# Performance work log

Measured on AMD Instinct MI355X. Metric: run time of the kernel, lower is better.

Reference implementation:

```python
import jax, jax.numpy as jnp
import numpy as np

N_HEADS = 16
PROJ_DIM = 64  # per-head dim
DIM = N_HEADS * PROJ_DIM  # 1024


def setup_inputs() -> dict:
    key = jax.random.key(0)
    k1, k2, k3, k4, k5 = jax.random.split(key, 5)
    N, L = 2, 2048
    scale = 1.0 / np.sqrt(DIM)
    return {
        "query": jax.random.normal(k1, (N, L, DIM), dtype=jnp.float32),
        "key": jax.random.normal(k2, (N, L, DIM), dtype=jnp.float32),
        "Wq": jax.random.normal(k3, (DIM, DIM), dtype=jnp.float32) * scale,
        "Wk": jax.random.normal(k4, (DIM, DIM), dtype=jnp.float32) * scale,
        "Wv": jax.random.normal(k5, (DIM, DIM), dtype=jnp.float32) * scale,
    }


def reference(query, key, Wq, Wk, Wv):
    # Causal linear-complexity attention (mask=True branch, left_first=False).
    N, Lq, _ = query.shape
    Lk = key.shape[1]
    H, Dh = N_HEADS, PROJ_DIM
    # torch Linear: x @ W.T ; reshape to (N, H, L, Dh)
    q = (query @ Wq.T).reshape(N, Lq, H, Dh).transpose(0, 2, 1, 3)
    k = (key @ Wk.T).reshape(N, Lk, H, Dh).transpose(0, 2, 1, 3)
    v = (key @ Wv.T).reshape(N, Lk, H, Dh).transpose(0, 2, 1, 3)
    q = jax.nn.softmax(q, axis=-1)
    k = jax.nn.softmax(k, axis=-1)
    # right[t] = sum_{s<=t} k_s^T v_s  : (N,H,Lk,Dh,Dh) cumulative outer products
    S = jnp.cumsum(jnp.einsum('nhti,nhtj->nhtij', k, v), axis=2)
    out = jnp.einsum('nhti,nhtij->nhtj', q, S)  # (N,H,Lq,Dh)
    return out.transpose(0, 2, 1, 3).reshape(N, Lq, H * Dh)
```

## Files before the change

### kernel.cpp

```cpp
#include <hip/hip_runtime.h>


constexpr int DIM  = 1024;
constexpr int H    = 16;
constexpr int DH   = 64;
constexpr int LSEQ = 2048;
constexpr int NB   = 2;
constexpr int MTOK = NB * LSEQ;
constexpr int CS   = 64;
constexpr int NC   = LSEQ / CS;
constexpr int SEG  = 8;
constexpr int CPS  = NC / SEG;

typedef __bf16 bf16x8 __attribute__((ext_vector_type(8)));
typedef float floatx4 __attribute__((ext_vector_type(4)));
typedef unsigned short ushort_t;

__device__ __forceinline__ ushort_t f2bf(float f) {
  unsigned int u = __float_as_uint(f);
  u += 0x7FFFu + ((u >> 16) & 1u);
  return (ushort_t)(u >> 16);
}

__device__ __forceinline__ void async16(void* lds, const void* g) {
  __builtin_amdgcn_global_load_lds(
      (const __attribute__((address_space(1))) unsigned int*)g,
      (__attribute__((address_space(3))) unsigned int*)lds, 16, 0, 0);
}

__device__ __forceinline__ bf16x8 tfrag(const unsigned int* T, int row, int uoff) {
  union { bf16x8 v; unsigned int u[4]; } r;
  const unsigned int* p = T + row * 33 + uoff;
  r.u[0] = p[0]; r.u[1] = p[1]; r.u[2] = p[2]; r.u[3] = p[3];
  return r.v;
}

__device__ __forceinline__ void transpose_tile(const ushort_t* g, unsigned int* TT, int tid) {
  const int ic = tid & 7, tp = tid >> 3;
  const ushort_t* r0 = g + (size_t)(2 * tp) * DIM + ic * 8;
  union { uint4 q; ushort_t u[8]; } a0, a1;
  a0.q = *(const uint4*)r0;
  a1.q = *(const uint4*)(r0 + DIM);
#pragma unroll
  for (int j = 0; j < 8; j++)
    TT[(8 * ic + j) * 33 + tp] = (unsigned int)a0.u[j] | ((unsigned int)a1.u[j] << 16);
}

__global__ __launch_bounds__(256) void cast_all(const float* __restrict__ q,
                                                const float* __restrict__ k,
                                                const float* __restrict__ wq,
                                                const float* __restrict__ wk,
                                                const float* __restrict__ wv,
                                                ushort_t* __restrict__ xbf,
                                                ushort_t* __restrict__ wbf) {
  const int seg = blockIdx.y;
  const float* src;
  ushort_t* dst;
  int n4;
  if (seg == 0)      { src = q;  dst = xbf;                  n4 = (4 << 20) / 4; }
  else if (seg == 1) { src = k;  dst = xbf + (4 << 20);      n4 = (4 << 20) / 4; }
  else if (seg == 2) { src = wq; dst = wbf;                  n4 = (1 << 20) / 4; }
  else if (seg == 3) { src = wk; dst = wbf + (1 << 20);      n4 = (1 << 20) / 4; }
  else               { src = wv; dst = wbf + (2 << 20);      n4 = (1 << 20) / 4; }
  for (int i = blockIdx.x * 256 + threadIdx.x; i < n4; i += gridDim.x * 256) {
    const float4 f = ((const float4*)src)[i];
    ((ushort4*)dst)[i] = make_ushort4(f2bf(f.x), f2bf(f.y), f2bf(f.z), f2bf(f.w));
  }
}

__global__ __launch_bounds__(512, 2) void gemm_fused(const ushort_t* __restrict__ xbf,
                                                     const ushort_t* __restrict__ wbf,
                                                     ushort_t* __restrict__ qp,
                                                     ushort_t* __restrict__ kp,
                                                     ushort_t* __restrict__ vp) {
  __shared__ __align__(16) ushort_t sh[65536];
  const int tid = threadIdx.x;

  const int xcd   = blockIdx.x & 7;
  const int local = blockIdx.x >> 3;
  const int T     = xcd * 24 + local;
  const int z     = T >> 6;
  const int rem   = T & 63;
  const int bm    = (rem >> 2) * 256;
  const int bn    = (rem & 3) * 256;

  const ushort_t* A = xbf + (z ? (size_t)(4 << 20) : 0);
  const ushort_t* W = wbf + (size_t)z * (1 << 20);
  ushort_t* C = (z == 0) ? qp : ((z == 1) ? kp : vp);

  const int lane  = tid & 63;
  const int wid   = tid >> 6;
  const int wr    = wid >> 2, wc = wid & 3;
  const int row16 = lane & 15, quad = lane >> 4;

  floatx4 acc[8][4] = {};

  const int srow = tid >> 3;
  const int lc   = (tid & 7) ^ (srow & 7);
  const ushort_t* pA[2][2];
  const ushort_t* pB[2][2];
#pragma unroll
  for (int h = 0; h < 2; h++)
#pragma unroll
    for (int rnd = 0; rnd < 2; rnd++) {
      pA[h][rnd] = A + (size_t)(bm + h * 128 + rnd * 64 + srow) * DIM + lc * 8;
      pB[h][rnd] = W + (size_t)(bn + h * 128 + rnd * 64 + srow) * DIM + lc * 8;
    }
  char* shW = (char*)sh;

#define STG(b, ism, h, kt)                                          \
  {                                                                 \
    char* d_ = shW + (b) * 65536 + (ism) * 32768 + (h) * 16384 + tid * 16; \
    async16(d_,        ((ism) ? pB : pA)[h][0] + (size_t)(kt) * 64);       \
    async16(d_ + 8192, ((ism) ? pB : pA)[h][1] + (size_t)(kt) * 64);       \
  }

  const int key = row16 & 7;
  const int xc0 = (quad ^ key) * 16;
  const int xc1 = ((4 + quad) ^ key) * 16;
  const int aOff = wr * 16384 + row16 * 128;
  const int bOff = 32768 + (wc >> 1) * 16384 + (wc & 1) * 8192 + row16 * 128;
  const char* shR = (const char*)sh;

  bf16x8 aF[4][2], bF[4][2];

#define RD_A4(p, base)                                                        \
  {                                                                           \
    _Pragma("unroll")                                                         \
    for (int mt = 0; mt < 4; mt++) {                                          \
      aF[mt][0] = *(const bf16x8*)(shR + (p) * 65536 + aOff + ((base) + mt) * 2048 + xc0); \
      aF[mt][1] = *(const bf16x8*)(shR + (p) * 65536 + aOff + ((base) + mt) * 2048 + xc1); \
    }                                                                         \
  }
#define RD_B2(p, base)                                                        \
  {                                                                           \
    _Pragma("unroll")                                                         \
    for (int j = 0; j < 2; j++) {                                             \
      bF[(base) + j][0] = *(const bf16x8*)(shR + (p) * 65536 + bOff + ((base) + j) * 2048 + xc0); \
      bF[(base) + j][1] = *(const bf16x8*)(shR + (p) * 65536 + bOff + ((base) + j) * 2048 + xc1); \
    }                                                                         \
  }
#define MFMA8(mb, nb)                                                         \
  {                                                                           \
    _Pragma("unroll")                                                         \
    for (int mt = 0; mt < 4; mt++)                                            \
      _Pragma("unroll")                                                       \
      for (int nt = 0; nt < 2; nt++) {                                        \
        acc[(mb) + mt][(nb) + nt] = __builtin_amdgcn_mfma_f32_16x16x32_bf16(  \
            aF[mt][0], bF[(nb) + nt][0], acc[(mb) + mt][(nb) + nt], 0, 0, 0); \
        acc[(mb) + mt][(nb) + nt] = __builtin_amdgcn_mfma_f32_16x16x32_bf16(  \
            aF[mt][1], bF[(nb) + nt][1], acc[(mb) + mt][(nb) + nt], 0, 0, 0); \
      }                                                                       \
  }
#define BARD()  asm volatile("s_barrier" ::: "memory")
#define LGKM0() asm volatile("s_waitcnt lgkmcnt(0)" ::: "memory")

  STG(0, 0, 0, 0); STG(0, 1, 0, 0);
  STG(0, 1, 1, 0); STG(0, 0, 1, 0);
  STG(1, 0, 0, 1); STG(1, 1, 0, 1);
  asm volatile("s_waitcnt vmcnt(4)" ::: "memory");
  BARD();

  for (int u = 0; u < 16; ++u) {
    const int p  = u & 1;
    const int qb = p ^ 1;
    RD_A4(p, 0); RD_B2(p, 0);
    if (u + 1 < 16) { STG(qb, 1, 1, u + 1); STG(qb, 0, 1, u + 1); }
    BARD(); LGKM0();
    __builtin_amdgcn_s_setprio(1); MFMA8(0, 0); __builtin_amdgcn_s_setprio(0);
    BARD();
    RD_B2(p, 2);
    BARD(); LGKM0();
    __builtin_amdgcn_s_setprio(1); MFMA8(0, 2); __builtin_amdgcn_s_setprio(0);
    BARD();
    RD_A4(p, 4);
    BARD(); LGKM0();
    __builtin_amdgcn_s_setprio(1); MFMA8(4, 0); __builtin_amdgcn_s_setprio(0);
    BARD();
    if (u + 2 < 16) {
      STG(p, 0, 0, u + 2); STG(p, 1, 0, u + 2);
      asm volatile("s_waitcnt vmcnt(4)" ::: "memory");
    } else {
      asm volatile("s_waitcnt vmcnt(0)" ::: "memory");
    }
    BARD();
    __builtin_amdgcn_s_setprio(1); MFMA8(4, 2); __builtin_amdgcn_s_setprio(0);
    BARD();
  }
#undef STG
#undef RD_A4
#undef RD_B2
#undef MFMA8
#undef BARD
#undef LGKM0
  __syncthreads();

  if (z < 2) {
#pragma unroll
    for (int mt = 0; mt < 8; mt++)
#pragma unroll
      for (int r = 0; r < 4; r++) {
        float m = fmaxf(fmaxf(acc[mt][0][r], acc[mt][1][r]),
                        fmaxf(acc[mt][2][r], acc[mt][3][r]));
#pragma unroll
        for (int o = 1; o < 16; o <<= 1) m = fmaxf(m, __shfl_xor(m, o, 64));
        float e[4], s = 0.f;
#pragma unroll
        for (int nt = 0; nt < 4; nt++) { e[nt] = __expf(acc[mt][nt][r] - m); s += e[nt]; }
#pragma unroll
        for (int o = 1; o < 16; o <<= 1) s += __shfl_xor(s, o, 64);
        const float inv = 1.f / s;
#pragma unroll
        for (int nt = 0; nt < 4; nt++) acc[mt][nt][r] = e[nt] * inv;
      }
  }

  ushort_t* CsB = sh;
#pragma unroll
  for (int p4 = 0; p4 < 4; ++p4) {
    __syncthreads();
    if (wr == (p4 >> 1)) {
      const int mh = (p4 & 1) * 4;
#pragma unroll
      for (int m4 = 0; m4 < 4; m4++)
#pragma unroll
        for (int nt = 0; nt < 4; nt++)
#pragma unroll
          for (int r = 0; r < 4; r++)
            CsB[(m4 * 16 + quad * 4 + r) * 264 + wc * 64 + nt * 16 + row16] =
                f2bf(acc[mh + m4][nt][r]);
    }
    __syncthreads();
#pragma unroll
    for (int it = 0; it < 4; it++) {
      const int ch = tid + it * 512;
      const int row = ch >> 5, ic = ch & 31;
      *(uint4*)&C[(size_t)(bm + p4 * 64 + row) * DIM + bn + ic * 8] =
          *(const uint4*)&CsB[row * 264 + ic * 8];
    }
  }
}

__global__ __launch_bounds__(1024, 1) void seg_T(const ushort_t* __restrict__ kp,
                                                 const ushort_t* __restrict__ vp,
                                                 float* __restrict__ cs,
                                                 float* __restrict__ segtot) {
  __shared__ unsigned int KT[4][64 * 33];
  __shared__ unsigned int VT[4][64 * 33];
  __shared__ float Tsl[3][DH * DH];
  const int s = blockIdx.x, h = blockIdx.y, n = blockIdx.z;
  const int tid = threadIdx.x;
  const int qd  = tid >> 8;
  const int t8  = tid & 255;
  const int lane = tid & 63;
  const int wid  = (tid >> 6) & 3;
  const int row16 = lane & 15, quad = lane >> 4;
  const int nh = n * H + h;
  const int c  = s * CPS + qd;
  const size_t gbase = ((size_t)(n * LSEQ + c * CS)) * DIM + h * DH;

  transpose_tile(kp + gbase, KT[qd], t8);
  transpose_tile(vp + gbase, VT[qd], t8);
  __syncthreads();

  floatx4 tacc[4] = {};
#pragma unroll
  for (int ks = 0; ks < 2; ks++) {
    const bf16x8 a = tfrag(VT[qd], wid * 16 + row16, ks * 16 + quad * 4);
#pragma unroll
    for (int nt = 0; nt < 4; nt++) {
      const bf16x8 b = tfrag(KT[qd], nt * 16 + row16, ks * 16 + quad * 4);
      tacc[nt] = __builtin_amdgcn_mfma_f32_16x16x32_bf16(a, b, tacc[nt], 0, 0, 0);
    }
  }
  if (qd < 3) {
#pragma unroll
    for (int nt = 0; nt < 4; nt++)
#pragma unroll
      for (int r = 0; r < 4; r++)
        Tsl[qd][(wid * 16 + quad * 4 + r) * DH + nt * 16 + row16] = tacc[nt][r];
  }
  __syncthreads();

  float* outp = cs + ((size_t)(nh * NC + c)) * (DH * DH);
#pragma unroll
  for (int nt = 0; nt < 4; nt++)
#pragma unroll
    for (int r = 0; r < 4; r++) {
      const int pos = (wid * 16 + quad * 4 + r) * DH + nt * 16 + row16;
      float p = 0.f;
      if (qd > 0) p += Tsl[0][pos];
      if (qd > 1) p += Tsl[1][pos];
      if (qd > 2) p += Tsl[2][pos];
      outp[pos] = p;
      if (qd == 3) {
        segtot[((size_t)(nh * SEG + s)) * (DH * DH) + pos] = p + tacc[nt][r];
      }
    }
}

__global__ __launch_bounds__(1024, 1) void attn2(const ushort_t* __restrict__ qp,
                                                 const ushort_t* __restrict__ kp,
                                                 const ushort_t* __restrict__ vp,
                                                 const float* __restrict__ cs,
                                                 const float* __restrict__ segtot,
                                                 float* __restrict__ out) {
  __shared__ ushort_t Qs[4][64 * 72];
  __shared__ ushort_t Ks[4][64 * 72];
  __shared__ ushort_t TsPb[4][64 * 72];
  __shared__ unsigned int VT2[4][64 * 33];
  const int s = blockIdx.x, h = blockIdx.y, n = blockIdx.z;
  const int tid = threadIdx.x;
  const int qd  = tid >> 8;
  const int t8  = tid & 255;
  const int lane = tid & 63;
  const int wl   = (tid >> 6) & 3;
  const int row16 = lane & 15, quad = lane >> 4;
  const int nh = n * H + h;
  const int c  = s * CPS + qd;
  const size_t gbase = ((size_t)(n * LSEQ + c * CS)) * DIM + h * DH;
  const float* Pc = cs + ((size_t)(nh * NC + c)) * (DH * DH);

  float sb[16] = {0.f, 0.f, 0.f, 0.f, 0.f, 0.f, 0.f, 0.f,
                  0.f, 0.f, 0.f, 0.f, 0.f, 0.f, 0.f, 0.f};
  {
    const float* base = segtot + (size_t)nh * SEG * (DH * DH);
    for (int sp = 0; sp < s; sp++) {
      const float* bsp = base + (size_t)sp * (DH * DH);
#pragma unroll
      for (int ii = 0; ii < 2; ii++) {
        const int e = (t8 + ii * 256) * 8;
        const float4 u0 = *(const float4*)(bsp + e);
        const float4 u1 = *(const float4*)(bsp + e + 4);
        sb[ii * 8 + 0] += u0.x; sb[ii * 8 + 1] += u0.y;
        sb[ii * 8 + 2] += u0.z; sb[ii * 8 + 3] += u0.w;
        sb[ii * 8 + 4] += u1.x; sb[ii * 8 + 5] += u1.y;
        sb[ii * 8 + 6] += u1.z; sb[ii * 8 + 7] += u1.w;
      }
    }
  }

#pragma unroll
  for (int it = 0; it < 2; it++) {
    const int ch = t8 + it * 256;
    const int row = ch >> 3, ic = ch & 7;
    *(uint4*)&Qs[qd][row * 72 + ic * 8] =
        *(const uint4*)&qp[gbase + (size_t)row * DIM + ic * 8];
    *(uint4*)&Ks[qd][row * 72 + ic * 8] =
        *(const uint4*)&kp[gbase + (size_t)row * DIM + ic * 8];
  }
  transpose_tile(vp + gbase, VT2[qd], t8);
#pragma unroll
  for (int ii = 0; ii < 2; ii++) {
    const int e = (t8 + ii * 256) * 8;
    const int row = e >> 6, col = e & 63;
    const float4 p0 = *(const float4*)(Pc + e);
    const float4 p1 = *(const float4*)(Pc + e + 4);
    ushort_t* d = &TsPb[qd][row * 72 + col];
    *(ushort4*)d = make_ushort4(
        f2bf(p0.x + sb[ii * 8 + 0]), f2bf(p0.y + sb[ii * 8 + 1]),
        f2bf(p0.z + sb[ii * 8 + 2]), f2bf(p0.w + sb[ii * 8 + 3]));
    *(ushort4*)(d + 4) = make_ushort4(
        f2bf(p1.x + sb[ii * 8 + 4]), f2bf(p1.y + sb[ii * 8 + 5]),
        f2bf(p1.z + sb[ii * 8 + 6]), f2bf(p1.w + sb[ii * 8 + 7]));
  }
  __syncthreads();

  const int t0 = wl * 16;
  floatx4 acc[4] = {};
  floatx4 pacc[4] = {};

#pragma unroll
  for (int ks = 0; ks < 2; ks++) {
    const bf16x8 aq = *(const bf16x8*)&Qs[qd][(t0 + row16) * 72 + ks * 32 + quad * 8];
#pragma unroll
    for (int nt = 0; nt < 4; nt++) {
      const bf16x8 bt = *(const bf16x8*)&TsPb[qd][(nt * 16 + row16) * 72 + ks * 32 + quad * 8];
      acc[nt] = __builtin_amdgcn_mfma_f32_16x16x32_bf16(aq, bt, acc[nt], 0, 0, 0);
      const bf16x8 bk = *(const bf16x8*)&Ks[qd][(nt * 16 + row16) * 72 + ks * 32 + quad * 8];
      pacc[nt] = __builtin_amdgcn_mfma_f32_16x16x32_bf16(aq, bk, pacc[nt], 0, 0, 0);
    }
  }
  __syncthreads();

#pragma unroll
  for (int nt = 0; nt < 4; nt++)
#pragma unroll
    for (int r = 0; r < 4; r++) {
      const int tt = t0 + quad * 4 + r, ss = nt * 16 + row16;
      TsPb[qd][tt * 72 + ss] = f2bf((ss <= tt) ? pacc[nt][r] : 0.f);
    }
  __syncthreads();

#pragma unroll
  for (int ks = 0; ks < 2; ks++) {
    const bf16x8 ap = *(const bf16x8*)&TsPb[qd][(t0 + row16) * 72 + ks * 32 + quad * 8];
#pragma unroll
    for (int nt = 0; nt < 4; nt++) {
      const bf16x8 bv = tfrag(VT2[qd], nt * 16 + row16, ks * 16 + quad * 4);
      acc[nt] = __builtin_amdgcn_mfma_f32_16x16x32_bf16(ap, bv, acc[nt], 0, 0, 0);
    }
  }

#pragma unroll
  for (int nt = 0; nt < 4; nt++)
#pragma unroll
    for (int r = 0; r < 4; r++)
      out[gbase + (size_t)(t0 + quad * 4 + r) * DIM + nt * 16 + row16] = acc[nt][r];
}

extern "C" void kernel_launch(void* const* d_in, const int* in_sizes, int n_in,
                              void* d_out, int out_size, void* d_ws, size_t ws_size,
                              hipStream_t stream) {
  const float* query = (const float*)d_in[0];
  const float* key   = (const float*)d_in[1];
  const float* Wq    = (const float*)d_in[2];
  const float* Wk    = (const float*)d_in[3];
  const float* Wv    = (const float*)d_in[4];
  float* out = (float*)d_out;

  const size_t PM = (size_t)4 << 20;
  ushort_t* qp = (ushort_t*)d_ws;
  ushort_t* kp = qp + PM;
  ushort_t* vp = kp + PM;
  float*    cs = (float*)(vp + PM);
  float*    segtot = cs + PM;
  ushort_t* xbf = (ushort_t*)cs;
  ushort_t* wbf = (ushort_t*)out;

  cast_all<<<dim3(512, 5), 256, 0, stream>>>(query, key, Wq, Wk, Wv, xbf, wbf);

  gemm_fused<<<dim3(192), 512, 0, stream>>>(xbf, wbf, qp, kp, vp);

  seg_T<<<dim3(SEG, H, NB), 1024, 0, stream>>>(kp, vp, cs, segtot);

  attn2<<<dim3(SEG, H, NB), 1024, 0, stream>>>(qp, kp, vp, cs, segtot, out);
}
```

Baseline: 160.3 us.

## Split attention into per-chunk 256-thread blocks and halve seg_T block size

The attention kernel now launches one 256-thread block per 64-token chunk instead of one 1024-thread block per segment of four chunks. It gets separate Ts and Pb buffers so one barrier can go. seg_T runs with 512 threads and loops twice over chunk pairs, with smaller LDS. The aim is more, smaller blocks for better occupancy and less LDS pressure per block, at the cost of each attention block re-reading the prefix segment totals.

```diff
diff --git a/kernel.cpp b/kernel.cpp
--- a/kernel.cpp
+++ b/kernel.cpp
@@ -241,83 +241,84 @@
   }
 }
 
-__global__ __launch_bounds__(1024, 1) void seg_T(const ushort_t* __restrict__ kp,
-                                                 const ushort_t* __restrict__ vp,
-                                                 float* __restrict__ cs,
-                                                 float* __restrict__ segtot) {
-  __shared__ unsigned int KT[4][64 * 33];
-  __shared__ unsigned int VT[4][64 * 33];
+__global__ __launch_bounds__(512) void seg_T(const ushort_t* __restrict__ kp,
+                                             const ushort_t* __restrict__ vp,
+                                             float* __restrict__ cs,
+                                             float* __restrict__ segtot) {
+  __shared__ unsigned int KT[2][64 * 33];
+  __shared__ unsigned int VT[2][64 * 33];
   __shared__ float Tsl[3][DH * DH];
   const int s = blockIdx.x, h = blockIdx.y, n = blockIdx.z;
   const int tid = threadIdx.x;
-  const int qd  = tid >> 8;
+  const int hf  = tid >> 8;
   const int t8  = tid & 255;
   const int lane = tid & 63;
   const int wid  = (tid >> 6) & 3;
   const int row16 = lane & 15, quad = lane >> 4;
   const int nh = n * H + h;
-  const int c  = s * CPS + qd;
-  const size_t gbase = ((size_t)(n * LSEQ + c * CS)) * DIM + h * DH;
-
-  transpose_tile(kp + gbase, KT[qd], t8);
-  transpose_tile(vp + gbase, VT[qd], t8);
-  __syncthreads();
-
-  floatx4 tacc[4] = {};
-#pragma unroll
-  for (int ks = 0; ks < 2; ks++) {
-    const bf16x8 a = tfrag(VT[qd], wid * 16 + row16, ks * 16 + quad * 4);
-#pragma unroll
-    for (int nt = 0; nt < 4; nt++) {
-      const bf16x8 b = tfrag(KT[qd], nt * 16 + row16, ks * 16 + quad * 4);
-      tacc[nt] = __builtin_amdgcn_mfma_f32_16x16x32_bf16(a, b, tacc[nt], 0, 0, 0);
-    }
-  }
-  if (qd < 3) {
+
+  for (int r = 0; r < 2; r++) {
+    const int idx = r * 2 + hf;
+    const int c   = s * CPS + idx;
+    const size_t gbase = ((size_t)(n * LSEQ + c * CS)) * DIM + h * DH;
+    if (r) __syncthreads();
+    transpose_tile(kp + gbase, KT[hf], t8);
+    transpose_tile(vp + gbase, VT[hf], t8);
+    __syncthreads();
+
+    floatx4 tacc[4] = {};
+#pragma unroll
+    for (int ks = 0; ks < 2; ks++) {
+      const bf16x8 a = tfrag(VT[hf], wid * 16 + row16, ks * 16 + quad * 4);
+#pragma unroll
+      for (int nt = 0; nt < 4; nt++) {
+        const bf16x8 b = tfrag(KT[hf], nt * 16 + row16, ks * 16 + quad * 4);
+        tacc[nt] = __builtin_amdgcn_mfma_f32_16x16x32_bf16(a, b, tacc[nt], 0, 0, 0);
+      }
+    }
+    if (idx < 3) {
+#pragma unroll
+      for (int nt = 0; nt < 4; nt++)
+#pragma unroll
+        for (int r4 = 0; r4 < 4; r4++)
+          Tsl[idx][(wid * 16 + quad * 4 + r4) * DH + nt * 16 + row16] = tacc[nt][r4];
+    }
+    __syncthreads();
+
+    float* outp = cs + ((size_t)(nh * NC + c)) * (DH * DH);
 #pragma unroll
     for (int nt = 0; nt < 4; nt++)
 #pragma unroll
-      for (int r = 0; r < 4; r++)
-        Tsl[qd][(wid * 16 + quad * 4 + r) * DH + nt * 16 + row16] = tacc[nt][r];
-  }
-  __syncthreads();
-
-  float* outp = cs + ((size_t)(nh * NC + c)) * (DH * DH);
-#pragma unroll
-  for (int nt = 0; nt < 4; nt++)
-#pragma unroll
-    for (int r = 0; r < 4; r++) {
-      const int pos = (wid * 16 + quad * 4 + r) * DH + nt * 16 + row16;
-      float p = 0.f;
-      if (qd > 0) p += Tsl[0][pos];
-      if (qd > 1) p += Tsl[1][pos];
-      if (qd > 2) p += Tsl[2][pos];
-      outp[pos] = p;
-      if (qd == 3) {
-        segtot[((size_t)(nh * SEG + s)) * (DH * DH) + pos] = p + tacc[nt][r];
+      for (int r4 = 0; r4 < 4; r4++) {
+        const int pos = (wid * 16 + quad * 4 + r4) * DH + nt * 16 + row16;
+        float p = 0.f;
+        if (idx > 0) p += Tsl[0][pos];
+        if (idx > 1) p += Tsl[1][pos];
+        if (idx > 2) p += Tsl[2][pos];
+        outp[pos] = p;
+        if (idx == 3)
+          segtot[((size_t)(nh * SEG + s)) * (DH * DH) + pos] = p + tacc[nt][r4];
       }
-    }
-}
-
-__global__ __launch_bounds__(1024, 1) void attn2(const ushort_t* __restrict__ qp,
-                                                 const ushort_t* __restrict__ kp,
-                                                 const ushort_t* __restrict__ vp,
-                                                 const float* __restrict__ cs,
-                                                 const float* __restrict__ segtot,
-                                                 float* __restrict__ out) {
-  __shared__ ushort_t Qs[4][64 * 72];
-  __shared__ ushort_t Ks[4][64 * 72];
-  __shared__ ushort_t TsPb[4][64 * 72];
-  __shared__ unsigned int VT2[4][64 * 33];
-  const int s = blockIdx.x, h = blockIdx.y, n = blockIdx.z;
+  }
+}
+
+__global__ __launch_bounds__(256) void attn3(const ushort_t* __restrict__ qp,
+                                             const ushort_t* __restrict__ kp,
+                                             const ushort_t* __restrict__ vp,
+                                             const float* __restrict__ cs,
+                                             const float* __restrict__ segtot,
+                                             float* __restrict__ out) {
+  __shared__ ushort_t Qs[64 * 72];
+  __shared__ ushort_t Ks[64 * 72];
+  __shared__ ushort_t Ts[64 * 72];
+  __shared__ ushort_t Pb[64 * 72];
+  __shared__ unsigned int VT[64 * 33];
+  const int c = blockIdx.x, h = blockIdx.y, n = blockIdx.z;
+  const int s = c >> 2;
   const int tid = threadIdx.x;
-  const int qd  = tid >> 8;
-  const int t8  = tid & 255;
-  const int lane = tid & 63;
-  const int wl   = (tid >> 6) & 3;
+  const int lane = tid & 63, wid = tid >> 6;
   const int row16 = lane & 15, quad = lane >> 4;
   const int nh = n * H + h;
-  const int c  = s * CPS + qd;
   const size_t gbase = ((size_t)(n * LSEQ + c * CS)) * DIM + h * DH;
   const float* Pc = cs + ((size_t)(nh * NC + c)) * (DH * DH);
 
@@ -329,7 +330,7 @@
       const float* bsp = base + (size_t)sp * (DH * DH);
 #pragma unroll
       for (int ii = 0; ii < 2; ii++) {
-        const int e = (t8 + ii * 256) * 8;
+        const int e = (tid + ii * 256) * 8;
         const float4 u0 = *(const float4*)(bsp + e);
         const float4 u1 = *(const float4*)(bsp + e + 4);
         sb[ii * 8 + 0] += u0.x; sb[ii * 8 + 1] += u0.y;
@@ -342,21 +343,19 @@
 
 #pragma unroll
   for (int it = 0; it < 2; it++) {
-    const int ch = t8 + it * 256;
+    const int ch = tid + it * 256;
     const int row = ch >> 3, ic = ch & 7;
-    *(uint4*)&Qs[qd][row * 72 + ic * 8] =
-        *(const uint4*)&qp[gbase + (size_t)row * DIM + ic * 8];
-    *(uint4*)&Ks[qd][row * 72 + ic * 8] =
-        *(const uint4*)&kp[gbase + (size_t)row * DIM + ic * 8];
-  }
-  transpose_tile(vp + gbase, VT2[qd], t8);
+    *(uint4*)&Qs[row * 72 + ic * 8] = *(const uint4*)&qp[gbase + (size_t)row * DIM + ic * 8];
+    *(uint4*)&Ks[row * 72 + ic * 8] = *(const uint4*)&kp[gbase + (size_t)row * DIM + ic * 8];
+  }
+  transpose_tile(vp + gbase, VT, tid);
 #pragma unroll
   for (int ii = 0; ii < 2; ii++) {
-    const int e = (t8 + ii * 256) * 8;
+    const int e = (tid + ii * 256) * 8;
     const int row = e >> 6, col = e & 63;
     const float4 p0 = *(const float4*)(Pc + e);
     const float4 p1 = *(const float4*)(Pc + e + 4);
-    ushort_t* d = &TsPb[qd][row * 72 + col];
+    ushort_t* d = &Ts[row * 72 + col];
     *(ushort4*)d = make_ushort4(
         f2bf(p0.x + sb[ii * 8 + 0]), f2bf(p0.y + sb[ii * 8 + 1]),
         f2bf(p0.z + sb[ii * 8 + 2]), f2bf(p0.w + sb[ii * 8 + 3]));
@@ -366,38 +365,36 @@
   }
   __syncthreads();
 
-  const int t0 = wl * 16;
+  const int t0 = wid * 16;
   floatx4 acc[4] = {};
   floatx4 pacc[4] = {};
 
 #pragma unroll
   for (int ks = 0; ks < 2; ks++) {
-    const bf16x8 aq = *(const bf16x8*)&Qs[qd][(t0 + row16) * 72 + ks * 32 + quad * 8];
+    const bf16x8 aq = *(const bf16x8*)&Qs[(t0 + row16) * 72 + ks * 32 + quad * 8];
 #pragma unroll
     for (int nt = 0; nt < 4; nt++) {
-      const bf16x8 bt = *(const bf16x8*)&TsPb[qd][(nt * 16 + row16) * 72 + ks * 32 + quad * 8];
+      const bf16x8 bt = *(const bf16x8*)&Ts[(nt * 16 + row16) * 72 + ks * 32 + quad * 8];
       acc[nt] = __builtin_amdgcn_mfma_f32_16x16x32_bf16(aq, bt, acc[nt], 0, 0, 0);
-      const bf16x8 bk = *(const bf16x8*)&Ks[qd][(nt * 16 + row16) * 72 + ks * 32 + quad * 8];
+      const bf16x8 bk = *(const bf16x8*)&Ks[(nt * 16 + row16) * 72 + ks * 32 + quad * 8];
       pacc[nt] = __builtin_amdgcn_mfma_f32_16x16x32_bf16(aq, bk, pacc[nt], 0, 0, 0);
     }
   }
-  __syncthreads();
-
 #pragma unroll
   for (int nt = 0; nt < 4; nt++)
 #pragma unroll
     for (int r = 0; r < 4; r++) {
       const int tt = t0 + quad * 4 + r, ss = nt * 16 + row16;
-      TsPb[qd][tt * 72 + ss] = f2bf((ss <= tt) ? pacc[nt][r] : 0.f);
+      Pb[tt * 72 + ss] = f2bf((ss <= tt) ? pacc[nt][r] : 0.f);
     }
   __syncthreads();
 
 #pragma unroll
   for (int ks = 0; ks < 2; ks++) {
-    const bf16x8 ap = *(const bf16x8*)&TsPb[qd][(t0 + row16) * 72 + ks * 32 + quad * 8];
+    const bf16x8 ap = *(const bf16x8*)&Pb[(t0 + row16) * 72 + ks * 32 + quad * 8];
 #pragma unroll
     for (int nt = 0; nt < 4; nt++) {
-      const bf16x8 bv = tfrag(VT2[qd], nt * 16 + row16, ks * 16 + quad * 4);
+      const bf16x8 bv = tfrag(VT, nt * 16 + row16, ks * 16 + quad * 4);
       acc[nt] = __builtin_amdgcn_mfma_f32_16x16x32_bf16(ap, bv, acc[nt], 0, 0, 0);
     }
   }
@@ -432,7 +429,7 @@
 
   gemm_fused<<<dim3(192), 512, 0, stream>>>(xbf, wbf, qp, kp, vp);
 
-  seg_T<<<dim3(SEG, H, NB), 1024, 0, stream>>>(kp, vp, cs, segtot);
-
-  attn2<<<dim3(SEG, H, NB), 1024, 0, stream>>>(qp, kp, vp, cs, segtot, out);
-}
+  seg_T<<<dim3(SEG, H, NB), 512, 0, stream>>>(kp, vp, cs, segtot);
+
+  attn3<<<dim3(NC, H, NB), 256, 0, stream>>>(qp, kp, vp, cs, segtot, out);
+}
```

Result: no change. 159.8 us (-0.3%).
